# Kernel optimization log

Measured on AMD Instinct MI355X. Metric: run time of the kernel, lower is better.

Reference implementation:

```python
import jax, jax.numpy as jnp
import numpy as np

T, B, INP, HID = 256, 128, 512, 512
LAST_K, RSIZE = 32, 64
ATTN = 1.0
NEG = -1e30  # stands in for float('-inf') in the mask; softmax weight is exactly 0 either way


def setup_inputs() -> dict:
    key = jax.random.key(0)
    ks = jax.random.split(key, 6)
    xav = lambda fi, fo: (2.0 / (fi + fo)) ** 0.5
    x = jax.random.normal(ks[0], (T, B, INP), jnp.float32)
    # torch Linear weights stored transposed so y = x @ W (+ b)
    Uw = jax.random.normal(ks[1], (INP, HID), jnp.float32) * xav(INP, HID)
    Ub = jnp.zeros((HID,), jnp.float32)
    Vw = jax.random.normal(ks[2], (HID, HID), jnp.float32) * xav(HID, HID)
    Uaw = jax.random.normal(ks[3], (HID, HID), jnp.float32) * xav(HID, HID)
    Vaw = jax.random.normal(ks[4], (HID, HID), jnp.float32) * xav(HID, HID)
    v = jax.random.normal(ks[5], (HID,), jnp.float32) * xav(1, HID)
    return {"x": x, "Uw": Uw, "Ub": Ub, "Vw": Vw, "Uaw": Uaw, "Vaw": Vaw, "v": v}


def reference(x, Uw, Ub, Vw, Uaw, Vaw, v):
    Tlen, Bsz, _ = x.shape
    H = Uw.shape[1]
    bidx = jnp.arange(Bsz)

    def step(carry, inp):
        xt, t = inp
        st, buf, slot_time, long_mem, long_mask, long_scores, buck, fcnt, lids = carry

        def first(_):
            # hidden is None -> zeros, so V(hidden) == 0; st is the pre-nonlinearity h
            pre = xt @ Uw + Ub
            return pre, jnp.tanh(pre), long_scores

        def later(_):
            va_st = st @ Vaw                                  # [B,H]
            # short-term memory attention (buf slot p holds h_{slot_time[p]}, -1 = empty)
            es = jnp.einsum('kbh,h->kb', jnp.tanh(va_st[None] + buf @ Uaw), v)
            es = jnp.where(slot_time[:, None] >= 0, es, NEG)  # mask empty slots
            es_l = jnp.einsum('rbh,h->rb', jnp.tanh(va_st[None] + long_mem @ Uaw), v) + long_mask
            alphas = jax.nn.softmax(jnp.concatenate([es, es_l], axis=0), axis=0)  # [K+R,B]
            comb = jnp.concatenate([buf, long_mem], axis=0)   # [K+R,B,H]
            ct = jnp.einsum('mb,mbh->bh', alphas, comb)
            last_h = buf[(t - 1) % LAST_K]                    # memory[-1] == h_{t-1}
            st_new = 0.5 * (last_h + ct * ATTN)
            h = jnp.tanh(xt @ Uw + Ub + st_new @ Vw)
            # detached accumulation of attention mass per timestep (long_scores[time] += alpha)
            det = jax.lax.stop_gradient(alphas[:LAST_K])
            valid = slot_time >= 0
            ls = long_scores.at[jnp.where(valid, slot_time, 0)].add(
                jnp.where(valid[:, None], det, 0.0))
            return st_new, h, ls

        st, h, long_scores = jax.lax.cond(t == 0, first, later, None)

        # --- conditional bucket eviction: candidate is h_{t-LAST_K} (oldest in buf) ---
        evict_step = t >= LAST_K
        cand = buf[t % LAST_K]                                # slot about to be overwritten
        score_t = long_scores[jnp.maximum(t - LAST_K, 0)]     # [B]
        minp = jnp.argmin(buck, axis=1)                       # [B]
        not_full = fcnt < RSIZE
        replace = score_t > buck[bidx, minp]
        do = evict_step & (not_full | replace)
        pos = jnp.where(not_full, fcnt, minp)                 # [B]
        long_mem = long_mem.at[pos, bidx].set(jnp.where(do[:, None], cand, long_mem[pos, bidx]))
        long_mask = long_mask.at[pos, bidx].set(jnp.where(do, 0.0, long_mask[pos, bidx]))
        buck = buck.at[bidx, pos].set(jnp.where(do, score_t, buck[bidx, pos]))
        lids = lids.at[bidx, pos].set(jnp.where(do, (t - LAST_K).astype(jnp.float32), lids[bidx, pos]))
        fcnt = jnp.where(do & not_full, fcnt + 1, fcnt)

        # append h to short-term circular buffer
        buf = buf.at[t % LAST_K].set(h)
        slot_time = slot_time.at[t % LAST_K].set(t)

        return (st, buf, slot_time, long_mem, long_mask, long_scores, buck, fcnt, lids), h

    carry0 = (
        jnp.zeros((Bsz, H), jnp.float32),                 # st
        jnp.zeros((LAST_K, Bsz, H), jnp.float32),         # short-term memory buffer
        -jnp.ones((LAST_K,), jnp.int32),                  # time stored in each buf slot
        jnp.zeros((RSIZE, Bsz, H), jnp.float32),          # long_mem buckets
        jnp.full((RSIZE, Bsz), NEG, jnp.float32),         # long_mask
        jnp.zeros((Tlen, Bsz), jnp.float32),              # long_scores
        jnp.zeros((Bsz, RSIZE), jnp.float32),             # buck_scores
        jnp.zeros((Bsz,), jnp.int32),                     # bucket fill count
        -jnp.ones((Bsz, RSIZE), jnp.float32),             # long_ids
    )
    _, hs = jax.lax.scan(step, carry0, (x, jnp.arange(Tlen)))
    return hs  # [T,B,H] hidden state at every step
```

## Files before the change

### kernel.cpp

```cpp
#include <hip/hip_runtime.h>
#include <hip/hip_bf16.h>
#include <cstddef>

#define kT 256
#define kB 128
#define kINP 512
#define kH 512
#define kK 32
#define kR 64
#define kNEG (-1e30f)

__device__ __forceinline__ void ag_store(float* p, float v) {
    __hip_atomic_store(p, v, __ATOMIC_RELAXED, __HIP_MEMORY_SCOPE_AGENT);
}
__device__ __forceinline__ float ag_load(const float* p) {
    return __hip_atomic_load(p, __ATOMIC_RELAXED, __HIP_MEMORY_SCOPE_AGENT);
}

__device__ __forceinline__ float ftanh(float x)
{
    float e = __expf(2.0f * x);
    return 1.0f - 2.0f * __builtin_amdgcn_rcpf(e + 1.0f);
}

__global__ __launch_bounds__(256) void gemm_xu(
    const float* __restrict__ A, const float* __restrict__ W,
    const float* __restrict__ bias, float* __restrict__ C)
{
    __shared__ float At[32][68];
    __shared__ float Ws[32][68];
    const int tid = threadIdx.x;
    const int n0 = blockIdx.x * 64;
    const int m0 = blockIdx.y * 64;
    const int tx = tid & 15, ty = tid >> 4;
    const int arow = tid >> 3, ak = (tid & 7) << 2;
    const int wrow = tid >> 4, wc = (tid & 15) << 2;

    float acc[4][4] = {};

    for (int k0 = 0; k0 < kINP; k0 += 32) {
        float4 a0 = *reinterpret_cast<const float4*>(&A[(size_t)(m0 + arow) * kINP + k0 + ak]);
        float4 a1 = *reinterpret_cast<const float4*>(&A[(size_t)(m0 + 32 + arow) * kINP + k0 + ak]);
        float4 w0 = *reinterpret_cast<const float4*>(&W[(size_t)(k0 + wrow) * kH + n0 + wc]);
        float4 w1 = *reinterpret_cast<const float4*>(&W[(size_t)(k0 + wrow + 16) * kH + n0 + wc]);
        __syncthreads();
        At[ak + 0][arow] = a0.x; At[ak + 1][arow] = a0.y;
        At[ak + 2][arow] = a0.z; At[ak + 3][arow] = a0.w;
        At[ak + 0][32 + arow] = a1.x; At[ak + 1][32 + arow] = a1.y;
        At[ak + 2][32 + arow] = a1.z; At[ak + 3][32 + arow] = a1.w;
        *reinterpret_cast<float4*>(&Ws[wrow][wc]) = w0;
        *reinterpret_cast<float4*>(&Ws[wrow + 16][wc]) = w1;
        __syncthreads();
#pragma unroll
        for (int kk = 0; kk < 32; ++kk) {
            float4 a4 = *reinterpret_cast<float4*>(&At[kk][ty * 4]);
            float4 w4 = *reinterpret_cast<float4*>(&Ws[kk][tx * 4]);
            float a_[4] = {a4.x, a4.y, a4.z, a4.w};
            float w_[4] = {w4.x, w4.y, w4.z, w4.w};
#pragma unroll
            for (int r = 0; r < 4; ++r)
#pragma unroll
                for (int c = 0; c < 4; ++c)
                    acc[r][c] += a_[r] * w_[c];
        }
    }

#pragma unroll
    for (int r = 0; r < 4; ++r) {
        int m = m0 + ty * 4 + r;
#pragma unroll
        for (int c = 0; c < 4; ++c) {
            int n = n0 + tx * 4 + c;
            C[(size_t)m * kH + n] = acc[r][c] + bias[n];
        }
    }
}

__global__ __launch_bounds__(256) void init_flags_k(int* __restrict__ flags)
{
    int i = blockIdx.x * 256 + threadIdx.x;
    if (i < kB * 3 * 2) flags[i] = 0;
}

__global__ __launch_bounds__(1024) void rnn_pair(
    const float* __restrict__ Vw, const float* __restrict__ Vaw,
    const float* __restrict__ Uaw, const float* __restrict__ vvec,
    const float* __restrict__ XU, float* __restrict__ lngU,
    float* __restrict__ hs, float* __restrict__ esx,
    float* __restrict__ stx, int* __restrict__ flags)
{
    extern __shared__ float dyn[];
    float* shortH = dyn;
    float* shortU = dyn + 32 * 256;
    float* longH  = dyn + 64 * 256;
    float* part   = dyn + 128 * 256;
    const int PSTR = 260;

    const int bid = blockIdx.x;
    const int b = bid >> 1, half = bid & 1;
    const int C0 = half << 8;
    const int P0 = (half ^ 1) << 8;
    const int tid = threadIdx.x;
    const int kq = tid >> 6;
    const int lane = tid & 63;
    const int c4 = lane << 2;

    __shared__ __align__(16) float h_sh[512];
    __shared__ __align__(16) float st_sh[512];
    __shared__ __align__(16) float va_sh[256];
    __shared__ __align__(16) float v_sh[256];
    __shared__ float es_own[96], es_sh[96];
    __shared__ int   rowm[96];
    __shared__ float lsc_sh[kT];
    __shared__ float buck_sh[kR];
    __shared__ int   lidx_sh[kR];
    __shared__ int   fcnt_sh, evict_pos;

    float* lngU_b = lngU + (size_t)bid * kR * 256;

    int* fC_own = &flags[(b * 3 + 0) * 2 + half];
    int* fB_own = &flags[(b * 3 + 1) * 2 + half];
    int* fS_own = &flags[(b * 3 + 2) * 2 + half];
    int* fC_par = &flags[(b * 3 + 0) * 2 + (half ^ 1)];
    int* fB_par = &flags[(b * 3 + 1) * 2 + (half ^ 1)];
    int* fS_par = &flags[(b * 3 + 2) * 2 + (half ^ 1)];

    auto wait_ge = [&](int* f, int target) {
        if (tid == 0) {
            while (__hip_atomic_load(f, __ATOMIC_RELAXED, __HIP_MEMORY_SCOPE_AGENT) < target)
                __builtin_amdgcn_s_sleep(1);
        }
        __syncthreads();
    };
    auto set_flag = [&](int* f, int val) {
        __syncthreads();
        if (tid == 0)
            __hip_atomic_store(f, val, __ATOMIC_RELAXED, __HIP_MEMORY_SCOPE_AGENT);
    };

    if (tid < 256) { v_sh[tid] = vvec[C0 + tid]; lsc_sh[tid] = 0.0f; }
    if (tid < kR) { buck_sh[tid] = 0.0f; lidx_sh[tid] = -1; }
    if (tid == 0) fcnt_sh = 0;
    if (tid < 512) st_sh[tid] = __builtin_nontemporal_load(&XU[(size_t)b * kH + tid]);
    __syncthreads();
    if (tid < 256) {
        float h0 = tanhf(st_sh[C0 + tid]);
        h_sh[C0 + tid] = h0;
        shortH[tid] = h0;
        ag_store(&hs[(size_t)b * kH + C0 + tid], h0);
    }
    set_flag(fC_own, 1);
    {
        float4 acc = {0, 0, 0, 0};
#pragma unroll 8
        for (int k = kq; k < kH; k += 16) {
            float s = st_sh[k];
            const float4 w = *reinterpret_cast<const float4*>(&Vaw[(size_t)k * kH + C0 + c4]);
            acc.x += s * w.x; acc.y += s * w.y; acc.z += s * w.z; acc.w += s * w.w;
        }
        *reinterpret_cast<float4*>(&part[kq * PSTR + c4]) = acc;
        __syncthreads();
        if (tid < 256) {
            float s = 0.0f;
#pragma unroll
            for (int j = 0; j < 16; ++j) s += part[j * PSTR + tid];
            va_sh[tid] = s;
        }
        __syncthreads();
    }

    for (int t = 1; t < kT; ++t) {
        float xu_reg = 0.0f;
        if (tid < 256)
            xu_reg = __builtin_nontemporal_load(&XU[((size_t)t * kB + b) * kH + C0 + tid]);

        float4 accA = {0, 0, 0, 0};
#pragma unroll 8
        for (int k = C0 + kq; k < C0 + 256; k += 16) {
            float s = h_sh[k];
            const float4 w = *reinterpret_cast<const float4*>(&Uaw[(size_t)k * kH + C0 + c4]);
            accA.x += s * w.x; accA.y += s * w.y; accA.z += s * w.z; accA.w += s * w.w;
        }
        if (tid < 96) {
            int row;
            if (tid < kK) { int md = (t + 31 - tid) & 31; row = t - 1 - md; }
            else row = lidx_sh[tid - kK];
            rowm[tid] = row;
        }
        wait_ge(fC_par, t);
        if (tid < 256) h_sh[P0 + tid] = ag_load(&hs[((size_t)(t - 1) * kB + b) * kH + P0 + tid]);
        __syncthreads();
#pragma unroll 8
        for (int k = P0 + kq; k < P0 + 256; k += 16) {
            float s = h_sh[k];
            const float4 w = *reinterpret_cast<const float4*>(&Uaw[(size_t)k * kH + C0 + c4]);
            accA.x += s * w.x; accA.y += s * w.y; accA.z += s * w.z; accA.w += s * w.w;
        }
        *reinterpret_cast<float4*>(&part[kq * PSTR + c4]) = accA;
        __syncthreads();
        if (tid < 256) {
            float u = 0.0f;
#pragma unroll
            for (int j = 0; j < 16; ++j) u += part[j * PSTR + tid];
            shortU[((t - 1) & 31) * 256 + tid] = u;
        }
        __syncthreads();

        {
            float4 uu[6];
            int rv[6];
#pragma unroll
            for (int r = 0; r < 6; ++r) {
                int m = kq + (r << 4);
                int row = rowm[m];
                rv[r] = row;
                uu[r] = make_float4(0.f, 0.f, 0.f, 0.f);
                if (row >= 0) {
                    const float* up = (m < kK) ? &shortU[m * 256]
                                               : &lngU_b[(size_t)(m - kK) * 256];
                    uu[r] = *reinterpret_cast<const float4*>(&up[c4]);
                }
            }
            const float4 vav = *reinterpret_cast<const float4*>(&va_sh[c4]);
            const float4 vvv = *reinterpret_cast<const float4*>(&v_sh[c4]);
#pragma unroll
            for (int r = 0; r < 6; ++r) {
                float p = 0.0f;
                if (rv[r] >= 0) {
                    p = vvv.x * ftanh(vav.x + uu[r].x) + vvv.y * ftanh(vav.y + uu[r].y)
                      + vvv.z * ftanh(vav.z + uu[r].z) + vvv.w * ftanh(vav.w + uu[r].w);
                }
#pragma unroll
                for (int off = 32; off; off >>= 1) p += __shfl_down(p, off);
                if (lane == 0) es_own[kq + (r << 4)] = p;
            }
        }
        __syncthreads();
        if (tid < 96) ag_store(&esx[((size_t)b * 2 + half) * 96 + tid], es_own[tid]);
        set_flag(fB_own, t);
        wait_ge(fB_par, t);
        if (tid < 96) {
            float e = kNEG;
            if (rowm[tid] >= 0)
                e = es_own[tid] + ag_load(&esx[((size_t)b * 2 + (half ^ 1)) * 96 + tid]);
            es_sh[tid] = e;
        }
        __syncthreads();

        float mx, inv;
        {
            float a = es_sh[lane];
            float b2 = (lane < 32) ? es_sh[64 + lane] : kNEG;
            float m2 = fmaxf(a, b2);
#pragma unroll
            for (int off = 32; off; off >>= 1) m2 = fmaxf(m2, __shfl_xor(m2, off));
            mx = m2;
            float e = __expf(a - mx) + ((lane < 32) ? __expf(b2 - mx) : 0.0f);
#pragma unroll
            for (int off = 32; off; off >>= 1) e += __shfl_xor(e, off);
            inv = 1.0f / e;
        }

        {
            float4 acc = {0, 0, 0, 0};
#pragma unroll
            for (int r = 0; r < 6; ++r) {
                int m = kq + (r << 4);
                int row = rowm[m];
                if (row >= 0) {
                    const float* hp = (m < kK) ? &shortH[m * 256]
                                               : &longH[(m - kK) * 256];
                    const float4 hv = *reinterpret_cast<const float4*>(&hp[c4]);
                    float wq = __expf(es_sh[m] - mx);
                    acc.x += wq * hv.x; acc.y += wq * hv.y;
                    acc.z += wq * hv.z; acc.w += wq * hv.w;
                }
            }
            *reinterpret_cast<float4*>(&part[kq * PSTR + c4]) = acc;
        }
        __syncthreads();
        if (tid < 256) {
            float ct = 0.0f;
#pragma unroll
            for (int j = 0; j < 16; ++j) ct += part[j * PSTR + tid];
            float stv = 0.5f * (h_sh[C0 + tid] + ct * inv);
            st_sh[C0 + tid] = stv;
            ag_store(&stx[(size_t)b * kH + C0 + tid], stv);
        }
        set_flag(fS_own, t);

        if (tid < kK) {
            int row = rowm[tid];
            if (row >= 0) lsc_sh[row] += __expf(es_sh[tid] - mx) * inv;
        }
        if (tid == 0) {
            int ep = -1;
            if (t >= kK) {
                float score = lsc_sh[t - kK];
                int fc = fcnt_sh;
                bool nf = fc < kR;
                float mn = buck_sh[0]; int mp = 0;
                for (int r = 1; r < kR; ++r) {
                    float bv = buck_sh[r];
                    if (bv < mn) { mn = bv; mp = r; }
                }
                if (nf || score > mn) {
                    ep = nf ? fc : mp;
                    lidx_sh[ep] = t - kK;
                    buck_sh[ep] = score;
                    if (nf) fcnt_sh = fc + 1;
                }
            }
            evict_pos = ep;
        }
        __syncthreads();
        if (evict_pos >= 0 && tid < 256) {
            longH[evict_pos * 256 + tid] = shortH[(t & 31) * 256 + tid];
            lngU_b[(size_t)evict_pos * 256 + tid] = shortU[(t & 31) * 256 + tid];
        }

        float4 aw4 = {0, 0, 0, 0};
#pragma unroll 8
        for (int k = C0 + kq; k < C0 + 256; k += 16) {
            float s = st_sh[k];
            const float4 w = *reinterpret_cast<const float4*>(&Vw[(size_t)k * kH + C0 + c4]);
            aw4.x += s * w.x; aw4.y += s * w.y; aw4.z += s * w.z; aw4.w += s * w.w;
        }
        wait_ge(fS_par, t);
        if (tid < 256) st_sh[P0 + tid] = ag_load(&stx[(size_t)b * kH + P0 + tid]);
        __syncthreads();
#pragma unroll 8
        for (int k = P0 + kq; k < P0 + 256; k += 16) {
            float s = st_sh[k];
            const float4 w = *reinterpret_cast<const float4*>(&Vw[(size_t)k * kH + C0 + c4]);
            aw4.x += s * w.x; aw4.y += s * w.y; aw4.z += s * w.z; aw4.w += s * w.w;
        }
        *reinterpret_cast<float4*>(&part[kq * PSTR + c4]) = aw4;
        __syncthreads();
        if (tid < 256) {
            float hpre = xu_reg;
#pragma unroll
            for (int j = 0; j < 16; ++j) hpre += part[j * PSTR + tid];
            float hval = tanhf(hpre);
            h_sh[C0 + tid] = hval;
            shortH[(t & 31) * 256 + tid] = hval;
            ag_store(&hs[((size_t)t * kB + b) * kH + C0 + tid], hval);
        }
        set_flag(fC_own, t + 1);

        {
            float4 av = {0, 0, 0, 0};
#pragma unroll 8
            for (int k = kq; k < kH; k += 16) {
                float s = st_sh[k];
                const float4 w = *reinterpret_cast<const float4*>(&Vaw[(size_t)k * kH + C0 + c4]);
                av.x += s * w.x; av.y += s * w.y; av.z += s * w.z; av.w += s * w.w;
            }
            *reinterpret_cast<float4*>(&part[kq * PSTR + c4]) = av;
        }
        __syncthreads();
        if (tid < 256) {
            float vn = 0.0f;
#pragma unroll
            for (int j = 0; j < 16; ++j) vn += part[j * PSTR + tid];
            va_sh[tid] = vn;
        }
        __syncthreads();
    }
}

extern "C" void kernel_launch(void* const* d_in, const int* in_sizes, int n_in,
                              void* d_out, int out_size, void* d_ws, size_t ws_size,
                              hipStream_t stream)
{
    const float* x   = (const float*)d_in[0];
    const float* Uw  = (const float*)d_in[1];
    const float* Ub  = (const float*)d_in[2];
    const float* Vw  = (const float*)d_in[3];
    const float* Uaw = (const float*)d_in[4];
    const float* Vaw = (const float*)d_in[5];
    const float* vv  = (const float*)d_in[6];
    float* hs = (float*)d_out;

    float* ws = (float*)d_ws;
    const size_t TBH = (size_t)kT * kB * kH;
    float* XU   = ws;
    float* lngU = XU + TBH;
    float* esx  = lngU + (size_t)2 * kB * kR * 256;
    float* stx  = esx + (size_t)kB * 2 * 96;
    int*   flags = (int*)(stx + (size_t)kB * kH);

    const int dyn_bytes = (32 * 256 + 32 * 256 + 64 * 256 + 16 * 260) * 4;
    hipFuncSetAttribute(reinterpret_cast<const void*>(rnn_pair),
                        hipFuncAttributeMaxDynamicSharedMemorySize, dyn_bytes);

    init_flags_k<<<3, 256, 0, stream>>>(flags);

    gemm_xu<<<dim3(kH / 64, (kT * kB) / 64), 256, 0, stream>>>(x, Uw, Ub, XU);

    rnn_pair<<<2 * kB, 1024, dyn_bytes, stream>>>(
        Vw, Vaw, Uaw, vv, XU, lngU, hs, esx, stx, flags);
}
```

Baseline: 6.692 ms.

## Compute softmax weights once in shared memory and adjust reduction padding

Softmax max, exponentials and inverse sum are now computed once by a single wavefront and stored in shared memory, instead of every wavefront redoing the reduction and recomputing exp per row. The weighted-sum loop now loads all values before accumulating. Nontemporal loads of XU become plain loads, and the partial-sum row stride changes from 260 to 264. The change adds several extra __syncthreads per timestep inside the serial recurrence, which may offset the saved exp work.

```diff
diff --git a/kernel.cpp b/kernel.cpp
--- a/kernel.cpp
+++ b/kernel.cpp
@@ -94,7 +94,7 @@
     float* shortU = dyn + 32 * 256;
     float* longH  = dyn + 64 * 256;
     float* part   = dyn + 128 * 256;
-    const int PSTR = 260;
+    const int PSTR = 264;
 
     const int bid = blockIdx.x;
     const int b = bid >> 1, half = bid & 1;
@@ -109,12 +109,13 @@
     __shared__ __align__(16) float st_sh[512];
     __shared__ __align__(16) float va_sh[256];
     __shared__ __align__(16) float v_sh[256];
-    __shared__ float es_own[96], es_sh[96];
+    __shared__ float es_own[96], es_sh[96], w_sh[96];
     __shared__ int   rowm[96];
     __shared__ float lsc_sh[kT];
     __shared__ float buck_sh[kR];
     __shared__ int   lidx_sh[kR];
     __shared__ int   fcnt_sh, evict_pos;
+    __shared__ float red0, red1;
 
     float* lngU_b = lngU + (size_t)bid * kR * 256;
 
@@ -141,7 +142,7 @@
     if (tid < 256) { v_sh[tid] = vvec[C0 + tid]; lsc_sh[tid] = 0.0f; }
     if (tid < kR) { buck_sh[tid] = 0.0f; lidx_sh[tid] = -1; }
     if (tid == 0) fcnt_sh = 0;
-    if (tid < 512) st_sh[tid] = __builtin_nontemporal_load(&XU[(size_t)b * kH + tid]);
+    if (tid < 512) st_sh[tid] = XU[(size_t)b * kH + tid];
     __syncthreads();
     if (tid < 256) {
         float h0 = tanhf(st_sh[C0 + tid]);
@@ -171,8 +172,7 @@
 
     for (int t = 1; t < kT; ++t) {
         float xu_reg = 0.0f;
-        if (tid < 256)
-            xu_reg = __builtin_nontemporal_load(&XU[((size_t)t * kB + b) * kH + C0 + tid]);
+        if (tid < 256) xu_reg = XU[((size_t)t * kB + b) * kH + C0 + tid];
 
         float4 accA = {0, 0, 0, 0};
 #pragma unroll 8
@@ -247,34 +247,44 @@
         }
         __syncthreads();
 
-        float mx, inv;
+        if (tid < 64) {
+            float a = es_sh[tid];
+            float c = (tid < 32) ? es_sh[64 + tid] : kNEG;
+            float mx = fmaxf(a, c);
+#pragma unroll
+            for (int off = 32; off; off >>= 1) mx = fmaxf(mx, __shfl_xor(mx, off));
+            if (tid == 0) red0 = mx;
+        }
+        __syncthreads();
+        if (tid < 96) w_sh[tid] = __expf(es_sh[tid] - red0);
+        __syncthreads();
+        if (tid < 64) {
+            float a = w_sh[tid] + ((tid < 32) ? w_sh[64 + tid] : 0.0f);
+#pragma unroll
+            for (int off = 32; off; off >>= 1) a += __shfl_xor(a, off);
+            if (tid == 0) red1 = 1.0f / a;
+        }
+        __syncthreads();
+
         {
-            float a = es_sh[lane];
-            float b2 = (lane < 32) ? es_sh[64 + lane] : kNEG;
-            float m2 = fmaxf(a, b2);
-#pragma unroll
-            for (int off = 32; off; off >>= 1) m2 = fmaxf(m2, __shfl_xor(m2, off));
-            mx = m2;
-            float e = __expf(a - mx) + ((lane < 32) ? __expf(b2 - mx) : 0.0f);
-#pragma unroll
-            for (int off = 32; off; off >>= 1) e += __shfl_xor(e, off);
-            inv = 1.0f / e;
-        }
-
-        {
-            float4 acc = {0, 0, 0, 0};
+            float4 hv[6]; float wq[6];
 #pragma unroll
             for (int r = 0; r < 6; ++r) {
                 int m = kq + (r << 4);
                 int row = rowm[m];
+                hv[r] = make_float4(0.f, 0.f, 0.f, 0.f); wq[r] = 0.0f;
                 if (row >= 0) {
                     const float* hp = (m < kK) ? &shortH[m * 256]
                                                : &longH[(m - kK) * 256];
-                    const float4 hv = *reinterpret_cast<const float4*>(&hp[c4]);
-                    float wq = __expf(es_sh[m] - mx);
-                    acc.x += wq * hv.x; acc.y += wq * hv.y;
-                    acc.z += wq * hv.z; acc.w += wq * hv.w;
+                    hv[r] = *reinterpret_cast<const float4*>(&hp[c4]);
+                    wq[r] = w_sh[m];
                 }
+            }
+            float4 acc = {0, 0, 0, 0};
+#pragma unroll
+            for (int r = 0; r < 6; ++r) {
+                acc.x += wq[r] * hv[r].x; acc.y += wq[r] * hv[r].y;
+                acc.z += wq[r] * hv[r].z; acc.w += wq[r] * hv[r].w;
             }
             *reinterpret_cast<float4*>(&part[kq * PSTR + c4]) = acc;
         }
@@ -283,7 +293,7 @@
             float ct = 0.0f;
 #pragma unroll
             for (int j = 0; j < 16; ++j) ct += part[j * PSTR + tid];
-            float stv = 0.5f * (h_sh[C0 + tid] + ct * inv);
+            float stv = 0.5f * (h_sh[C0 + tid] + ct * red1);
             st_sh[C0 + tid] = stv;
             ag_store(&stx[(size_t)b * kH + C0 + tid], stv);
         }
@@ -291,8 +301,9 @@
 
         if (tid < kK) {
             int row = rowm[tid];
-            if (row >= 0) lsc_sh[row] += __expf(es_sh[tid] - mx) * inv;
-        }
+            if (row >= 0) lsc_sh[row] += w_sh[tid] * red1;
+        }
+        __syncthreads();
         if (tid == 0) {
             int ep = -1;
             if (t >= kK) {
@@ -319,32 +330,34 @@
             lngU_b[(size_t)evict_pos * 256 + tid] = shortU[(t & 31) * 256 + tid];
         }
 
-        float4 aw4 = {0, 0, 0, 0};
-#pragma unroll 8
-        for (int k = C0 + kq; k < C0 + 256; k += 16) {
-            float s = st_sh[k];
-            const float4 w = *reinterpret_cast<const float4*>(&Vw[(size_t)k * kH + C0 + c4]);
-            aw4.x += s * w.x; aw4.y += s * w.y; aw4.z += s * w.z; aw4.w += s * w.w;
-        }
-        wait_ge(fS_par, t);
-        if (tid < 256) st_sh[P0 + tid] = ag_load(&stx[(size_t)b * kH + P0 + tid]);
-        __syncthreads();
-#pragma unroll 8
-        for (int k = P0 + kq; k < P0 + 256; k += 16) {
-            float s = st_sh[k];
-            const float4 w = *reinterpret_cast<const float4*>(&Vw[(size_t)k * kH + C0 + c4]);
-            aw4.x += s * w.x; aw4.y += s * w.y; aw4.z += s * w.z; aw4.w += s * w.w;
-        }
-        *reinterpret_cast<float4*>(&part[kq * PSTR + c4]) = aw4;
+        {
+            float4 aw = {0, 0, 0, 0};
+#pragma unroll 8
+            for (int k = C0 + kq; k < C0 + 256; k += 16) {
+                float s = st_sh[k];
+                const float4 w = *reinterpret_cast<const float4*>(&Vw[(size_t)k * kH + C0 + c4]);
+                aw.x += s * w.x; aw.y += s * w.y; aw.z += s * w.z; aw.w += s * w.w;
+            }
+            wait_ge(fS_par, t);
+            if (tid < 256) st_sh[P0 + tid] = ag_load(&stx[(size_t)b * kH + P0 + tid]);
+            __syncthreads();
+#pragma unroll 8
+            for (int k = P0 + kq; k < P0 + 256; k += 16) {
+                float s = st_sh[k];
+                const float4 w = *reinterpret_cast<const float4*>(&Vw[(size_t)k * kH + C0 + c4]);
+                aw.x += s * w.x; aw.y += s * w.y; aw.z += s * w.z; aw.w += s * w.w;
+            }
+            *reinterpret_cast<float4*>(&part[kq * PSTR + c4]) = aw;
+        }
         __syncthreads();
         if (tid < 256) {
             float hpre = xu_reg;
 #pragma unroll
             for (int j = 0; j < 16; ++j) hpre += part[j * PSTR + tid];
-            float hval = tanhf(hpre);
-            h_sh[C0 + tid] = hval;
-            shortH[(t & 31) * 256 + tid] = hval;
-            ag_store(&hs[((size_t)t * kB + b) * kH + C0 + tid], hval);
+            float hv = tanhf(hpre);
+            h_sh[C0 + tid] = hv;
+            shortH[(t & 31) * 256 + tid] = hv;
+            ag_store(&hs[((size_t)t * kB + b) * kH + C0 + tid], hv);
         }
         set_flag(fC_own, t + 1);
 
@@ -390,7 +403,7 @@
     float* stx  = esx + (size_t)kB * 2 * 96;
     int*   flags = (int*)(stx + (size_t)kB * kH);
 
-    const int dyn_bytes = (32 * 256 + 32 * 256 + 64 * 256 + 16 * 260) * 4;
+    const int dyn_bytes = (32 * 256 + 32 * 256 + 64 * 256 + 16 * 264) * 4;
     hipFuncSetAttribute(reinterpret_cast<const void*>(rnn_pair),
                         hipFuncAttributeMaxDynamicSharedMemorySize, dyn_bytes);
 
```

New measurement: 5.658 ms. -15.4%, faster.
